# Performance work log

Hardware: AMD Instinct MI355X
Metric: run time of the kernel (lower is better)

The kernel has to match this reference:

```python
import jax, jax.numpy as jnp
import numpy as np

K = 14  # kernel_size == stride (non-overlapping patches)


def setup_inputs() -> dict:
    key = jax.random.key(0)
    k1, k2, k3, k4, k5 = jax.random.split(key, 5)
    b, c, h, w = 4, 384, 224, 224
    H, W = h // K, w // K  # final_size = (16, 16)
    hr_feats = jax.random.normal(k1, (b, c, h, w), dtype=jnp.float32)
    guidance = jnp.zeros((1,), dtype=jnp.float32)  # unused by forward()
    # attention_net: Dropout (eval=identity) -> Linear(dim, 1)
    attn_w = jax.random.normal(k2, (1, c), dtype=jnp.float32) * (1.0 / np.sqrt(c))
    attn_b = jnp.zeros((1,), dtype=jnp.float32)
    # learned per-position affine over the k*k patch axis
    w_kk = jnp.ones((K, K), dtype=jnp.float32) + 0.01 * jax.random.normal(k3, (K, K), dtype=jnp.float32)
    b_kk = jnp.zeros((K, K), dtype=jnp.float32) + 0.01 * jax.random.normal(k4, (K, K), dtype=jnp.float32)
    # forward-time dropout mask: torch.rand(b,H,W,1) > 0.2
    dropout_mask = jax.random.uniform(k5, (b, H, W, 1)) > 0.2
    return {"hr_feats": hr_feats, "guidance": guidance, "attn_w": attn_w,
            "attn_b": attn_b, "w_kk": w_kk, "b_kk": b_kk,
            "dropout_mask": dropout_mask}


def reference(hr_feats, guidance, attn_w, attn_b, w_kk, b_kk, dropout_mask):
    b, c, h, w = hr_feats.shape
    H, W = h // K, w // K
    # Unfold with stride == kernel_size: non-overlapping patches via reshape.
    # (b,c,h,w) -> (b,c,H,K,W,K) -> (b,H,W,K,K,c) -> (b,H,W,p=K*K,c)
    patches = hr_feats.reshape(b, c, H, K, W, K).transpose(0, 2, 4, 3, 5, 1)
    patches = patches.reshape(b, H, W, K * K, c)
    # tiny linear scorer: (b,H,W,p,c) @ (c,) -> (b,H,W,p)
    patch_logits = jnp.einsum('bhwpc,c->bhwp', patches, attn_w[0]) + attn_b[0]
    mask = dropout_mask.astype(patch_logits.dtype)  # (b,H,W,1)
    logits = patch_logits * mask * w_kk.reshape(-1) + b_kk.reshape(-1)
    attn = jax.nn.softmax(logits, axis=-1)  # over the p = K*K patch axis
    # softmax-weighted patch reduction
    downsampled = jnp.einsum('bhwpc,bhwp->bchw', patches, attn)
    return downsampled  # (b, c, H, W); slice [:, :c] is identity here
```

## Files before the change

kernel.cpp:

```cpp
#include <hip/hip_runtime.h>
#include <math.h>

#define B 4
#define C 384
#define HIN 224
#define WIN 224
#define KS 14
#define HB 16
#define WBL 16
#define P 196

__global__ __launch_bounds__(256) void k_rowsum(const float* __restrict__ hr,
                                                const float* __restrict__ attn_w,
                                                float* __restrict__ rowsum) {
    __shared__ float wlds[C];
    __shared__ float4 red[224];
    const int blk = blockIdx.x;
    const int b = blk / HIN, h = blk % HIN;
    const int tid = threadIdx.x;
    for (int i = tid; i < C; i += 256) wlds[i] = attn_w[i];
    __syncthreads();

    const int wave = tid >> 6, lane = tid & 63;
    float4 acc = make_float4(0.f, 0.f, 0.f, 0.f);
    if (lane < 56) {
        const float* base = hr + (size_t)b * C * (HIN * WIN) + (size_t)h * WIN + lane * 4;
        for (int c = wave; c < C; c += 4) {
            const float4 v = *reinterpret_cast<const float4*>(base + (size_t)c * (HIN * WIN));
            const float wc = wlds[c];
            acc.x += v.x * wc; acc.y += v.y * wc; acc.z += v.z * wc; acc.w += v.w * wc;
        }
        red[wave * 56 + lane] = acc;
    }
    __syncthreads();
    if (tid < 56) {
        const float4 a0 = red[tid], a1 = red[56 + tid], a2 = red[112 + tid], a3 = red[168 + tid];
        float4 s;
        s.x = a0.x + a1.x + a2.x + a3.x;
        s.y = a0.y + a1.y + a2.y + a3.y;
        s.z = a0.z + a1.z + a2.z + a3.z;
        s.w = a0.w + a1.w + a2.w + a3.w;
        reinterpret_cast<float4*>(rowsum + (size_t)blk * WIN)[tid] = s;
    }
}

__global__ __launch_bounds__(256) void k_softmax(const float* __restrict__ rowsum,
                                                 const float* __restrict__ attn_b,
                                                 const float* __restrict__ w_kk,
                                                 const float* __restrict__ b_kk,
                                                 const int* __restrict__ mask,
                                                 float* __restrict__ attn) {
    const int blk = blockIdx.x;
    const int wb = blk % WBL;
    const int hb = (blk / WBL) % HB;
    const int b = blk / (WBL * HB);
    const int tid = threadIdx.x;

    float logit = 0.f;
    float l = -INFINITY;
    if (tid < P) {
        const int ki = tid / KS, kj = tid % KS;
        const float rv = rowsum[((size_t)b * HIN + hb * KS + ki) * WIN + wb * KS + kj];
        const float m = mask[(b * HB + hb) * WBL + wb] ? 1.f : 0.f;
        logit = (rv + attn_b[0]) * m * w_kk[tid] + b_kk[tid];
        l = logit;
    }

    __shared__ float smax[4], ssum[4];
    float v = l;
    #pragma unroll
    for (int off = 32; off; off >>= 1) v = fmaxf(v, __shfl_xor(v, off));
    if ((tid & 63) == 0) smax[tid >> 6] = v;
    __syncthreads();
    const float bm = fmaxf(fmaxf(smax[0], smax[1]), fmaxf(smax[2], smax[3]));

    float e = (tid < P) ? expf(logit - bm) : 0.f;
    float s = e;
    #pragma unroll
    for (int off = 32; off; off >>= 1) s += __shfl_xor(s, off);
    if ((tid & 63) == 0) ssum[tid >> 6] = s;
    __syncthreads();
    const float bs = ssum[0] + ssum[1] + ssum[2] + ssum[3];

    if (tid < P) attn[(size_t)blk * P + tid] = e / bs;
}

__global__ __launch_bounds__(256) void k_weighted(const float* __restrict__ hr,
                                                  const float* __restrict__ attn,
                                                  float* __restrict__ out) {
    __shared__ float alds[WBL * P];
    __shared__ float colsum[WIN];
    const int blk = blockIdx.x;
    const int hb = blk % HB;
    const int c = (blk / HB) % C;
    const int b = blk / (HB * C);
    const int tid = threadIdx.x;

    const float* abase = attn + ((size_t)b * HB + hb) * WBL * P;
    for (int i = tid; i < WBL * P; i += 256) alds[i] = abase[i];
    __syncthreads();

    if (tid < WIN) {
        const int wb = tid / KS, kj = tid % KS;
        const float* hbase = hr + ((size_t)(b * C + c) * HIN + hb * KS) * WIN + tid;
        const float* arow = alds + wb * P + kj;
        float acc = 0.f;
        #pragma unroll
        for (int ki = 0; ki < KS; ++ki)
            acc += hbase[(size_t)ki * WIN] * arow[ki * KS];
        colsum[tid] = acc;
    }
    __syncthreads();
    if (tid < WBL) {
        float s = 0.f;
        #pragma unroll
        for (int kj = 0; kj < KS; ++kj) s += colsum[tid * KS + kj];
        out[((size_t)(b * C + c) * HB + hb) * WBL + tid] = s;
    }
}

extern "C" void kernel_launch(void* const* d_in, const int* in_sizes, int n_in,
                              void* d_out, int out_size, void* d_ws, size_t ws_size,
                              hipStream_t stream) {
    const float* hr      = (const float*)d_in[0];
    const float* attn_w  = (const float*)d_in[2];
    const float* attn_b  = (const float*)d_in[3];
    const float* w_kk    = (const float*)d_in[4];
    const float* b_kk    = (const float*)d_in[5];
    const int*   mask    = (const int*)d_in[6];
    float* out = (float*)d_out;

    float* rowsum = (float*)d_ws;
    float* attn   = rowsum + (size_t)B * HIN * WIN;

    k_rowsum<<<B * HIN, 256, 0, stream>>>(hr, attn_w, rowsum);
    k_softmax<<<B * HB * WBL, 256, 0, stream>>>(rowsum, attn_b, w_kk, b_kk, mask, attn);
    k_weighted<<<B * C * HB, 256, 0, stream>>>(hr, attn, out);
}
```

Before: 127.3 us.

## Process per batch to reuse cache and fuse softmax into weighted reduction

Splits work per batch image so the second pass over hr_feats reads data still resident in cache after the rowsum pass. The rowsum is split into four channel groups whose partial sums are combined in the fused kernel. The softmax is computed inside the weighted-reduction kernel, with each block handling 8 channels, which removes the attn buffer and one launch. In exchange there are more kernel launches and smaller grids, and the per-channel loop in the fused kernel is serialized with barriers.

```diff
diff --git a/kernel.cpp b/kernel.cpp
--- a/kernel.cpp
+++ b/kernel.cpp
@@ -9,28 +9,34 @@
 #define HB 16
 #define WBL 16
 #define P 196
+#define HW (HIN * WIN)
+#define CG 4
+#define CPG (C / CG)
+#define NC 8
 
-__global__ __launch_bounds__(256) void k_rowsum(const float* __restrict__ hr,
-                                                const float* __restrict__ attn_w,
-                                                float* __restrict__ rowsum) {
-    __shared__ float wlds[C];
+__global__ __launch_bounds__(256) void k_rowsum_b(const float* __restrict__ hr_b,
+                                                  const float* __restrict__ attn_w,
+                                                  float* __restrict__ part) {
+    __shared__ float wlds[CPG];
     __shared__ float4 red[224];
     const int blk = blockIdx.x;
-    const int b = blk / HIN, h = blk % HIN;
+    const int h = blk % HIN, g = blk / HIN;
     const int tid = threadIdx.x;
-    for (int i = tid; i < C; i += 256) wlds[i] = attn_w[i];
+    if (tid < CPG) wlds[tid] = attn_w[g * CPG + tid];
     __syncthreads();
 
-    const int wave = tid >> 6, lane = tid & 63;
+    const int wv = tid >> 6, lane = tid & 63;
     float4 acc = make_float4(0.f, 0.f, 0.f, 0.f);
     if (lane < 56) {
-        const float* base = hr + (size_t)b * C * (HIN * WIN) + (size_t)h * WIN + lane * 4;
-        for (int c = wave; c < C; c += 4) {
-            const float4 v = *reinterpret_cast<const float4*>(base + (size_t)c * (HIN * WIN));
-            const float wc = wlds[c];
+        const float* base = hr_b + (size_t)(g * CPG) * HW + (size_t)h * WIN + lane * 4;
+        #pragma unroll 4
+        for (int j = 0; j < CPG / 4; ++j) {
+            const int cl = wv + 4 * j;
+            const float4 v = *reinterpret_cast<const float4*>(base + (size_t)cl * HW);
+            const float wc = wlds[cl];
             acc.x += v.x * wc; acc.y += v.y * wc; acc.z += v.z * wc; acc.w += v.w * wc;
         }
-        red[wave * 56 + lane] = acc;
+        red[wv * 56 + lane] = acc;
     }
     __syncthreads();
     if (tid < 56) {
@@ -40,82 +46,91 @@
         s.y = a0.y + a1.y + a2.y + a3.y;
         s.z = a0.z + a1.z + a2.z + a3.z;
         s.w = a0.w + a1.w + a2.w + a3.w;
-        reinterpret_cast<float4*>(rowsum + (size_t)blk * WIN)[tid] = s;
+        reinterpret_cast<float4*>(part + ((size_t)g * HIN + h) * WIN)[tid] = s;
     }
 }
 
-__global__ __launch_bounds__(256) void k_softmax(const float* __restrict__ rowsum,
+__global__ __launch_bounds__(256) void k_fused_b(const float* __restrict__ hr_b,
+                                                 const float* __restrict__ part,
                                                  const float* __restrict__ attn_b,
                                                  const float* __restrict__ w_kk,
                                                  const float* __restrict__ b_kk,
-                                                 const int* __restrict__ mask,
-                                                 float* __restrict__ attn) {
-    const int blk = blockIdx.x;
-    const int wb = blk % WBL;
-    const int hb = (blk / WBL) % HB;
-    const int b = blk / (WBL * HB);
+                                                 const int* __restrict__ mask_b,
+                                                 float* __restrict__ out_b) {
+    __shared__ float e_lds[KS * WIN];
+    __shared__ float wkk[P], bkk[P];
+    __shared__ float colsum[2][WIN];
+    __shared__ float wbmax[WBL], wbsum[WBL], maskv[WBL];
+    const int hb = blockIdx.x & 15;
+    const int cg = blockIdx.x >> 4;
     const int tid = threadIdx.x;
 
-    float logit = 0.f;
-    float l = -INFINITY;
-    if (tid < P) {
-        const int ki = tid / KS, kj = tid % KS;
-        const float rv = rowsum[((size_t)b * HIN + hb * KS + ki) * WIN + wb * KS + kj];
-        const float m = mask[(b * HB + hb) * WBL + wb] ? 1.f : 0.f;
-        logit = (rv + attn_b[0]) * m * w_kk[tid] + b_kk[tid];
-        l = logit;
-    }
-
-    __shared__ float smax[4], ssum[4];
-    float v = l;
-    #pragma unroll
-    for (int off = 32; off; off >>= 1) v = fmaxf(v, __shfl_xor(v, off));
-    if ((tid & 63) == 0) smax[tid >> 6] = v;
-    __syncthreads();
-    const float bm = fmaxf(fmaxf(smax[0], smax[1]), fmaxf(smax[2], smax[3]));
-
-    float e = (tid < P) ? expf(logit - bm) : 0.f;
-    float s = e;
-    #pragma unroll
-    for (int off = 32; off; off >>= 1) s += __shfl_xor(s, off);
-    if ((tid & 63) == 0) ssum[tid >> 6] = s;
-    __syncthreads();
-    const float bs = ssum[0] + ssum[1] + ssum[2] + ssum[3];
-
-    if (tid < P) attn[(size_t)blk * P + tid] = e / bs;
-}
-
-__global__ __launch_bounds__(256) void k_weighted(const float* __restrict__ hr,
-                                                  const float* __restrict__ attn,
-                                                  float* __restrict__ out) {
-    __shared__ float alds[WBL * P];
-    __shared__ float colsum[WIN];
-    const int blk = blockIdx.x;
-    const int hb = blk % HB;
-    const int c = (blk / HB) % C;
-    const int b = blk / (HB * C);
-    const int tid = threadIdx.x;
-
-    const float* abase = attn + ((size_t)b * HB + hb) * WBL * P;
-    for (int i = tid; i < WBL * P; i += 256) alds[i] = abase[i];
+    if (tid < P) { wkk[tid] = w_kk[tid]; bkk[tid] = b_kk[tid]; }
+    if (tid >= 224 && tid < 240) maskv[tid - 224] = mask_b[hb * WBL + (tid - 224)] ? 1.f : 0.f;
     __syncthreads();
 
+    const float ab = attn_b[0];
+    for (int i = tid; i < KS * WIN; i += 256) {
+        const int ki = i / WIN, w = i % WIN;
+        const int wb = w / KS, kj = w % KS;
+        const float r = part[((size_t)0 * HIN + hb * KS + ki) * WIN + w]
+                      + part[((size_t)1 * HIN + hb * KS + ki) * WIN + w]
+                      + part[((size_t)2 * HIN + hb * KS + ki) * WIN + w]
+                      + part[((size_t)3 * HIN + hb * KS + ki) * WIN + w];
+        const int p = ki * KS + kj;
+        e_lds[i] = (r + ab) * maskv[wb] * wkk[p] + bkk[p];
+    }
+    __syncthreads();
     if (tid < WIN) {
-        const int wb = tid / KS, kj = tid % KS;
-        const float* hbase = hr + ((size_t)(b * C + c) * HIN + hb * KS) * WIN + tid;
-        const float* arow = alds + wb * P + kj;
-        float acc = 0.f;
+        float m = -INFINITY;
         #pragma unroll
-        for (int ki = 0; ki < KS; ++ki)
-            acc += hbase[(size_t)ki * WIN] * arow[ki * KS];
-        colsum[tid] = acc;
+        for (int ki = 0; ki < KS; ++ki) m = fmaxf(m, e_lds[ki * WIN + tid]);
+        colsum[0][tid] = m;
+    }
+    __syncthreads();
+    if (tid < WBL) {
+        float m = -INFINITY;
+        #pragma unroll
+        for (int kj = 0; kj < KS; ++kj) m = fmaxf(m, colsum[0][tid * KS + kj]);
+        wbmax[tid] = m;
+    }
+    __syncthreads();
+    for (int i = tid; i < KS * WIN; i += 256) {
+        const int wb = (i % WIN) / KS;
+        e_lds[i] = __expf(e_lds[i] - wbmax[wb]);
+    }
+    __syncthreads();
+    if (tid < WIN) {
+        float s = 0.f;
+        #pragma unroll
+        for (int ki = 0; ki < KS; ++ki) s += e_lds[ki * WIN + tid];
+        colsum[0][tid] = s;
     }
     __syncthreads();
     if (tid < WBL) {
         float s = 0.f;
         #pragma unroll
-        for (int kj = 0; kj < KS; ++kj) s += colsum[tid * KS + kj];
-        out[((size_t)(b * C + c) * HB + hb) * WBL + tid] = s;
+        for (int kj = 0; kj < KS; ++kj) s += colsum[0][tid * KS + kj];
+        wbsum[tid] = s;
+    }
+    __syncthreads();
+    for (int n = 0; n < NC; ++n) {
+        const int c = cg * NC + n;
+        const float* hbase = hr_b + ((size_t)c * HIN + hb * KS) * WIN;
+        if (tid < WIN) {
+            float acc = 0.f;
+            #pragma unroll
+            for (int ki = 0; ki < KS; ++ki)
+                acc += hbase[(size_t)ki * WIN + tid] * e_lds[ki * WIN + tid];
+            colsum[n & 1][tid] = acc;
+        }
+        __syncthreads();
+        if (tid < WBL) {
+            float s = 0.f;
+            #pragma unroll
+            for (int kj = 0; kj < KS; ++kj) s += colsum[n & 1][tid * KS + kj];
+            out_b[(size_t)c * (HB * WBL) + hb * WBL + tid] = s / wbsum[tid];
+        }
     }
 }
 
@@ -130,10 +145,13 @@
     const int*   mask    = (const int*)d_in[6];
     float* out = (float*)d_out;
 
-    float* rowsum = (float*)d_ws;
-    float* attn   = rowsum + (size_t)B * HIN * WIN;
+    float* part = (float*)d_ws;
 
-    k_rowsum<<<B * HIN, 256, 0, stream>>>(hr, attn_w, rowsum);
-    k_softmax<<<B * HB * WBL, 256, 0, stream>>>(rowsum, attn_b, w_kk, b_kk, mask, attn);
-    k_weighted<<<B * C * HB, 256, 0, stream>>>(hr, attn, out);
+    for (int b = 0; b < B; ++b) {
+        const float* hr_b = hr + (size_t)b * C * HW;
+        k_rowsum_b<<<HIN * CG, 256, 0, stream>>>(hr_b, attn_w, part);
+        k_fused_b<<<HB * (C / NC), 256, 0, stream>>>(hr_b, part, attn_b, w_kk, b_kk,
+                                                     mask + b * HB * WBL,
+                                                     out + (size_t)b * C * HB * WBL);
+    }
 }
```

Result: slower. 135.3 us (+6.3%).

## Split channel reduction across blocks and reuse attention tiles over channel groups

Applied to the files above, without the earlier changes.

The logit GEMV now tiles the flattened spatial plane into 1024-element chunks and splits channels into two groups that write partial sums, which the softmax kernel adds together. The weighted-reduction kernel loads each attention tile into LDS once, laid out as spatial rows, and reuses it across 8 channels with float4 loads. This replaces one block per (b,c,hb) that reloaded the same attention tile. The aim is fewer redundant attention loads and better-vectorized streaming of the large input, at the cost of extra partial-sum traffic and more syncs inside each block. Softmax also switches to the fast __expf.

```diff
diff --git a/kernel.cpp b/kernel.cpp
--- a/kernel.cpp
+++ b/kernel.cpp
@@ -9,42 +9,35 @@
 #define HB 16
 #define WBL 16
 #define P 196
+#define HW (HIN * WIN)
+#define CG 2
+#define CPG (C / CG)
+#define NT 49
+#define NC 8
 
-__global__ __launch_bounds__(256) void k_rowsum(const float* __restrict__ hr,
-                                                const float* __restrict__ attn_w,
-                                                float* __restrict__ rowsum) {
-    __shared__ float wlds[C];
-    __shared__ float4 red[224];
-    const int blk = blockIdx.x;
-    const int b = blk / HIN, h = blk % HIN;
+__global__ __launch_bounds__(256) void k_gemv(const float* __restrict__ hr,
+                                              const float* __restrict__ attn_w,
+                                              float* __restrict__ part) {
+    __shared__ float wlds[CPG];
     const int tid = threadIdx.x;
-    for (int i = tid; i < C; i += 256) wlds[i] = attn_w[i];
+    const int cg = blockIdx.x & 1;
+    const int t  = (blockIdx.x >> 1) % NT;
+    const int b  = blockIdx.x / (2 * NT);
+    if (tid < CPG) wlds[tid] = attn_w[cg * CPG + tid];
     __syncthreads();
 
-    const int wave = tid >> 6, lane = tid & 63;
+    const float* base = hr + (size_t)(b * C + cg * CPG) * HW + t * 1024 + tid * 4;
     float4 acc = make_float4(0.f, 0.f, 0.f, 0.f);
-    if (lane < 56) {
-        const float* base = hr + (size_t)b * C * (HIN * WIN) + (size_t)h * WIN + lane * 4;
-        for (int c = wave; c < C; c += 4) {
-            const float4 v = *reinterpret_cast<const float4*>(base + (size_t)c * (HIN * WIN));
-            const float wc = wlds[c];
-            acc.x += v.x * wc; acc.y += v.y * wc; acc.z += v.z * wc; acc.w += v.w * wc;
-        }
-        red[wave * 56 + lane] = acc;
+    #pragma unroll 8
+    for (int c = 0; c < CPG; ++c) {
+        const float4 v = *reinterpret_cast<const float4*>(base + (size_t)c * HW);
+        const float wc = wlds[c];
+        acc.x += v.x * wc; acc.y += v.y * wc; acc.z += v.z * wc; acc.w += v.w * wc;
     }
-    __syncthreads();
-    if (tid < 56) {
-        const float4 a0 = red[tid], a1 = red[56 + tid], a2 = red[112 + tid], a3 = red[168 + tid];
-        float4 s;
-        s.x = a0.x + a1.x + a2.x + a3.x;
-        s.y = a0.y + a1.y + a2.y + a3.y;
-        s.z = a0.z + a1.z + a2.z + a3.z;
-        s.w = a0.w + a1.w + a2.w + a3.w;
-        reinterpret_cast<float4*>(rowsum + (size_t)blk * WIN)[tid] = s;
-    }
+    reinterpret_cast<float4*>(part + (size_t)(b * CG + cg) * HW + t * 1024)[tid] = acc;
 }
 
-__global__ __launch_bounds__(256) void k_softmax(const float* __restrict__ rowsum,
+__global__ __launch_bounds__(256) void k_softmax(const float* __restrict__ part,
                                                  const float* __restrict__ attn_b,
                                                  const float* __restrict__ w_kk,
                                                  const float* __restrict__ b_kk,
@@ -60,7 +53,9 @@
     float l = -INFINITY;
     if (tid < P) {
         const int ki = tid / KS, kj = tid % KS;
-        const float rv = rowsum[((size_t)b * HIN + hb * KS + ki) * WIN + wb * KS + kj];
+        const size_t idx = (size_t)(hb * KS + ki) * WIN + wb * KS + kj;
+        const float rv = part[(size_t)(b * CG + 0) * HW + idx]
+                       + part[(size_t)(b * CG + 1) * HW + idx];
         const float m = mask[(b * HB + hb) * WBL + wb] ? 1.f : 0.f;
         logit = (rv + attn_b[0]) * m * w_kk[tid] + b_kk[tid];
         l = logit;
@@ -74,7 +69,7 @@
     __syncthreads();
     const float bm = fmaxf(fmaxf(smax[0], smax[1]), fmaxf(smax[2], smax[3]));
 
-    float e = (tid < P) ? expf(logit - bm) : 0.f;
+    float e = (tid < P) ? __expf(logit - bm) : 0.f;
     float s = e;
     #pragma unroll
     for (int off = 32; off; off >>= 1) s += __shfl_xor(s, off);
@@ -88,34 +83,51 @@
 __global__ __launch_bounds__(256) void k_weighted(const float* __restrict__ hr,
                                                   const float* __restrict__ attn,
                                                   float* __restrict__ out) {
-    __shared__ float alds[WBL * P];
+    __shared__ float e_lds[KS * WIN];
+    __shared__ float4 red4[224];
     __shared__ float colsum[WIN];
-    const int blk = blockIdx.x;
-    const int hb = blk % HB;
-    const int c = (blk / HB) % C;
-    const int b = blk / (HB * C);
     const int tid = threadIdx.x;
+    const int cg = blockIdx.x % 48;
+    const int hb = (blockIdx.x / 48) & 15;
+    const int b  = blockIdx.x / (48 * 16);
 
-    const float* abase = attn + ((size_t)b * HB + hb) * WBL * P;
-    for (int i = tid; i < WBL * P; i += 256) alds[i] = abase[i];
+    const float* abase = attn + (size_t)((b * HB + hb) * WBL) * P;
+    for (int i = tid; i < WBL * P; i += 256) {
+        const int wb = i / P, p = i % P;
+        e_lds[(p / KS) * WIN + wb * KS + (p % KS)] = abase[i];
+    }
     __syncthreads();
 
-    if (tid < WIN) {
-        const int wb = tid / KS, kj = tid % KS;
-        const float* hbase = hr + ((size_t)(b * C + c) * HIN + hb * KS) * WIN + tid;
-        const float* arow = alds + wb * P + kj;
-        float acc = 0.f;
-        #pragma unroll
-        for (int ki = 0; ki < KS; ++ki)
-            acc += hbase[(size_t)ki * WIN] * arow[ki * KS];
-        colsum[tid] = acc;
-    }
-    __syncthreads();
-    if (tid < WBL) {
-        float s = 0.f;
-        #pragma unroll
-        for (int kj = 0; kj < KS; ++kj) s += colsum[tid * KS + kj];
-        out[((size_t)(b * C + c) * HB + hb) * WBL + tid] = s;
+    const int ki0 = tid / 56, fc = tid % 56;
+    for (int n = 0; n < NC; ++n) {
+        const int c = cg * NC + n;
+        const float* hbase = hr + (size_t)((b * C + c) * HIN + hb * KS) * WIN;
+        if (tid < 224) {
+            float4 acc = make_float4(0.f, 0.f, 0.f, 0.f);
+            #pragma unroll
+            for (int r = ki0; r < KS; r += 4) {
+                const float4 v = *reinterpret_cast<const float4*>(hbase + r * WIN + fc * 4);
+                const float4 e = *reinterpret_cast<const float4*>(e_lds + r * WIN + fc * 4);
+                acc.x += v.x * e.x; acc.y += v.y * e.y;
+                acc.z += v.z * e.z; acc.w += v.w * e.w;
+            }
+            red4[tid] = acc;
+        }
+        __syncthreads();
+        if (tid < 56) {
+            const float4 a0 = red4[tid], a1 = red4[56 + tid],
+                         a2 = red4[112 + tid], a3 = red4[168 + tid];
+            reinterpret_cast<float4*>(colsum)[tid] = make_float4(
+                a0.x + a1.x + a2.x + a3.x, a0.y + a1.y + a2.y + a3.y,
+                a0.z + a1.z + a2.z + a3.z, a0.w + a1.w + a2.w + a3.w);
+        }
+        __syncthreads();
+        if (tid < WBL) {
+            float s = 0.f;
+            #pragma unroll
+            for (int kj = 0; kj < KS; ++kj) s += colsum[tid * KS + kj];
+            out[(size_t)((b * C + c) * HB + hb) * WBL + tid] = s;
+        }
     }
 }
 
@@ -130,10 +142,10 @@
     const int*   mask    = (const int*)d_in[6];
     float* out = (float*)d_out;
 
-    float* rowsum = (float*)d_ws;
-    float* attn   = rowsum + (size_t)B * HIN * WIN;
+    float* part = (float*)d_ws;
+    float* attn = part + (size_t)B * CG * HW;
 
-    k_rowsum<<<B * HIN, 256, 0, stream>>>(hr, attn_w, rowsum);
-    k_softmax<<<B * HB * WBL, 256, 0, stream>>>(rowsum, attn_b, w_kk, b_kk, mask, attn);
-    k_weighted<<<B * C * HB, 256, 0, stream>>>(hr, attn, out);
+    k_gemv<<<B * NT * CG, 256, 0, stream>>>(hr, attn_w, part);
+    k_softmax<<<B * HB * WBL, 256, 0, stream>>>(part, attn_b, w_kk, b_kk, mask, attn);
+    k_weighted<<<B * 16 * 48, 256, 0, stream>>>(hr, attn, out);
 }
```

Result: faster. 109.5 us (-13.9%).

## Fuse scorer, softmax and weighted reduction into one kernel with bf16 LDS patch

Applied to the files above, without the earlier changes.

Replaces the three-kernel pipeline with one kernel per output patch. The kernel loads all channels of the 14x14 patch into LDS as packed bf16, computes logits, softmax and the weighted channel reduction from LDS. This avoids reading the input twice from HBM and drops the workspace round-trips. In exchange it loses input precision to bf16 and needs a large LDS footprint that limits occupancy, and its global loads are short strided rows.

```diff
diff --git a/kernel.cpp b/kernel.cpp
--- a/kernel.cpp
+++ b/kernel.cpp
@@ -9,113 +9,101 @@
 #define HB 16
 #define WBL 16
 #define P 196
+#define ROWDW 101
 
-__global__ __launch_bounds__(256) void k_rowsum(const float* __restrict__ hr,
-                                                const float* __restrict__ attn_w,
-                                                float* __restrict__ rowsum) {
+__device__ __forceinline__ unsigned int f2bf(float f) {
+    union { float f; unsigned int u; } c; c.f = f;
+    return (c.u + 0x7fffu + ((c.u >> 16) & 1u)) >> 16;
+}
+__device__ __forceinline__ float bf2f(unsigned int bits16) {
+    union { unsigned int u; float f; } c; c.u = bits16 << 16;
+    return c.f;
+}
+
+__global__ __launch_bounds__(512, 2) void k_fused(const float* __restrict__ hr,
+                                                  const float* __restrict__ attn_w,
+                                                  const float* __restrict__ attn_b,
+                                                  const float* __restrict__ w_kk,
+                                                  const float* __restrict__ b_kk,
+                                                  const int* __restrict__ mask,
+                                                  float* __restrict__ out) {
+    __shared__ unsigned int x4[C * ROWDW];
+    __shared__ __align__(8) float e_lds[200];
     __shared__ float wlds[C];
-    __shared__ float4 red[224];
+    __shared__ float plds[392];
+    __shared__ float smax[8], ssum[8];
+    const int tid = threadIdx.x;
     const int blk = blockIdx.x;
-    const int b = blk / HIN, h = blk % HIN;
-    const int tid = threadIdx.x;
-    for (int i = tid; i < C; i += 256) wlds[i] = attn_w[i];
+    const int wb = blk & 15, hb = (blk >> 4) & 15, b = blk >> 8;
+
+    if (tid < C) wlds[tid] = attn_w[tid];
+
+    if (tid < C) {
+        const float* src = hr + ((size_t)(b * C + tid) * HIN + hb * KS) * WIN + wb * KS;
+        unsigned int* xrow = x4 + tid * ROWDW;
+        #pragma unroll
+        for (int ki = 0; ki < KS; ++ki) {
+            const float2* r = reinterpret_cast<const float2*>(src + (size_t)ki * WIN);
+            #pragma unroll
+            for (int j = 0; j < 7; ++j) {
+                const float2 v = r[j];
+                xrow[ki * 7 + j] = f2bf(v.x) | (f2bf(v.y) << 16);
+            }
+        }
+    }
     __syncthreads();
 
-    const int wave = tid >> 6, lane = tid & 63;
-    float4 acc = make_float4(0.f, 0.f, 0.f, 0.f);
-    if (lane < 56) {
-        const float* base = hr + (size_t)b * C * (HIN * WIN) + (size_t)h * WIN + lane * 4;
-        for (int c = wave; c < C; c += 4) {
-            const float4 v = *reinterpret_cast<const float4*>(base + (size_t)c * (HIN * WIN));
-            const float wc = wlds[c];
-            acc.x += v.x * wc; acc.y += v.y * wc; acc.z += v.z * wc; acc.w += v.w * wc;
+    if (tid < 392) {
+        const int p = tid % P, cs = tid / P;
+        const int dj = p >> 1, sh = (p & 1) << 4;
+        const int c0 = cs * 192;
+        float part = 0.f;
+        #pragma unroll 8
+        for (int c = c0; c < c0 + 192; ++c) {
+            const unsigned int u = x4[c * ROWDW + dj];
+            part += bf2f((u >> sh) & 0xffffu) * wlds[c];
         }
-        red[wave * 56 + lane] = acc;
+        plds[tid] = part;
     }
     __syncthreads();
-    if (tid < 56) {
-        const float4 a0 = red[tid], a1 = red[56 + tid], a2 = red[112 + tid], a3 = red[168 + tid];
-        float4 s;
-        s.x = a0.x + a1.x + a2.x + a3.x;
-        s.y = a0.y + a1.y + a2.y + a3.y;
-        s.z = a0.z + a1.z + a2.z + a3.z;
-        s.w = a0.w + a1.w + a2.w + a3.w;
-        reinterpret_cast<float4*>(rowsum + (size_t)blk * WIN)[tid] = s;
-    }
-}
 
-__global__ __launch_bounds__(256) void k_softmax(const float* __restrict__ rowsum,
-                                                 const float* __restrict__ attn_b,
-                                                 const float* __restrict__ w_kk,
-                                                 const float* __restrict__ b_kk,
-                                                 const int* __restrict__ mask,
-                                                 float* __restrict__ attn) {
-    const int blk = blockIdx.x;
-    const int wb = blk % WBL;
-    const int hb = (blk / WBL) % HB;
-    const int b = blk / (WBL * HB);
-    const int tid = threadIdx.x;
-
-    float logit = 0.f;
     float l = -INFINITY;
     if (tid < P) {
-        const int ki = tid / KS, kj = tid % KS;
-        const float rv = rowsum[((size_t)b * HIN + hb * KS + ki) * WIN + wb * KS + kj];
+        const float rv = plds[tid] + plds[P + tid];
         const float m = mask[(b * HB + hb) * WBL + wb] ? 1.f : 0.f;
-        logit = (rv + attn_b[0]) * m * w_kk[tid] + b_kk[tid];
-        l = logit;
+        l = (rv + attn_b[0]) * m * w_kk[tid] + b_kk[tid];
     }
 
-    __shared__ float smax[4], ssum[4];
     float v = l;
     #pragma unroll
     for (int off = 32; off; off >>= 1) v = fmaxf(v, __shfl_xor(v, off));
     if ((tid & 63) == 0) smax[tid >> 6] = v;
     __syncthreads();
-    const float bm = fmaxf(fmaxf(smax[0], smax[1]), fmaxf(smax[2], smax[3]));
+    float bm = smax[0];
+    #pragma unroll
+    for (int k = 1; k < 8; ++k) bm = fmaxf(bm, smax[k]);
 
-    float e = (tid < P) ? expf(logit - bm) : 0.f;
+    const float e = (tid < P) ? __expf(l - bm) : 0.f;
     float s = e;
     #pragma unroll
     for (int off = 32; off; off >>= 1) s += __shfl_xor(s, off);
     if ((tid & 63) == 0) ssum[tid >> 6] = s;
+    if (tid < P) e_lds[tid] = e;
     __syncthreads();
-    const float bs = ssum[0] + ssum[1] + ssum[2] + ssum[3];
+    const float S = ((ssum[0] + ssum[1]) + (ssum[2] + ssum[3]))
+                  + ((ssum[4] + ssum[5]) + (ssum[6] + ssum[7]));
 
-    if (tid < P) attn[(size_t)blk * P + tid] = e / bs;
-}
-
-__global__ __launch_bounds__(256) void k_weighted(const float* __restrict__ hr,
-                                                  const float* __restrict__ attn,
-                                                  float* __restrict__ out) {
-    __shared__ float alds[WBL * P];
-    __shared__ float colsum[WIN];
-    const int blk = blockIdx.x;
-    const int hb = blk % HB;
-    const int c = (blk / HB) % C;
-    const int b = blk / (HB * C);
-    const int tid = threadIdx.x;
-
-    const float* abase = attn + ((size_t)b * HB + hb) * WBL * P;
-    for (int i = tid; i < WBL * P; i += 256) alds[i] = abase[i];
-    __syncthreads();
-
-    if (tid < WIN) {
-        const int wb = tid / KS, kj = tid % KS;
-        const float* hbase = hr + ((size_t)(b * C + c) * HIN + hb * KS) * WIN + tid;
-        const float* arow = alds + wb * P + kj;
+    if (tid < C) {
+        const unsigned int* xrow = x4 + tid * ROWDW;
+        const float2* e2 = reinterpret_cast<const float2*>(e_lds);
         float acc = 0.f;
-        #pragma unroll
-        for (int ki = 0; ki < KS; ++ki)
-            acc += hbase[(size_t)ki * WIN] * arow[ki * KS];
-        colsum[tid] = acc;
-    }
-    __syncthreads();
-    if (tid < WBL) {
-        float s = 0.f;
-        #pragma unroll
-        for (int kj = 0; kj < KS; ++kj) s += colsum[tid * KS + kj];
-        out[((size_t)(b * C + c) * HB + hb) * WBL + tid] = s;
+        #pragma unroll 14
+        for (int d = 0; d < 98; ++d) {
+            const unsigned int u = xrow[d];
+            const float2 ee = e2[d];
+            acc += ee.x * bf2f(u & 0xffffu) + ee.y * bf2f(u >> 16);
+        }
+        out[((size_t)(b * C + tid) * HB + hb) * WBL + wb] = acc / S;
     }
 }
 
@@ -130,10 +118,5 @@
     const int*   mask    = (const int*)d_in[6];
     float* out = (float*)d_out;
 
-    float* rowsum = (float*)d_ws;
-    float* attn   = rowsum + (size_t)B * HIN * WIN;
-
-    k_rowsum<<<B * HIN, 256, 0, stream>>>(hr, attn_w, rowsum);
-    k_softmax<<<B * HB * WBL, 256, 0, stream>>>(rowsum, attn_b, w_kk, b_kk, mask, attn);
-    k_weighted<<<B * C * HB, 256, 0, stream>>>(hr, attn, out);
+    k_fused<<<B * HB * WBL, 512, 0, stream>>>(hr, attn_w, attn_b, w_kk, b_kk, mask, out);
 }
```

New measurement: 171.2 us. +34.5%, slower.
